# Optimization experiments

Hardware: AMD Instinct MI355X
Metric: run time of the kernel (lower is better)

## Reference

```python
import jax, jax.numpy as jnp
import numpy as np

B, T, D_IN, H, K, C = 8, 2048, 512, 384, 8192, 8
N_BLOCKS = 6
EPS = 1e-5


def conv1d(x, w, b, pad, groups=1):
    # x: [B, Cin, T], w: [Cout, Cin//groups, k]
    y = jax.lax.conv_general_dilated(
        x, w, window_strides=(1,), padding=[(pad, pad)],
        dimension_numbers=("NCH", "OIH", "NCH"), feature_group_count=groups)
    return y + b[None, :, None]


def layernorm(x, g, b):
    # normalize over last axis
    m = jnp.mean(x, axis=-1, keepdims=True)
    v = jnp.mean(jnp.square(x - m), axis=-1, keepdims=True)
    return (x - m) * jax.lax.rsqrt(v + EPS) * g + b


def setup_inputs() -> dict:
    key = jax.random.key(0)
    ks = iter(jax.random.split(key, 32))
    s = 0.02
    inp = {
        "x": jax.random.normal(next(ks), (B, T, D_IN), dtype=jnp.float32),
        "enc_w": jax.random.normal(next(ks), (H, D_IN, 7)) * s,
        "enc_b": jnp.zeros((H,)),
        "enc_ln_g": jnp.ones((H,)),
        "enc_ln_b": jnp.zeros((H,)),
        "blk_dw_w": jax.random.normal(next(ks), (N_BLOCKS, H, 1, 7)) * s,
        "blk_dw_b": jnp.zeros((N_BLOCKS, H)),
        "blk_ln_g": jnp.ones((N_BLOCKS, H)),
        "blk_ln_b": jnp.zeros((N_BLOCKS, H)),
        "blk_w1": jax.random.normal(next(ks), (N_BLOCKS, 4 * H, H)) * s,
        "blk_b1": jnp.zeros((N_BLOCKS, 4 * H)),
        "blk_w2": jax.random.normal(next(ks), (N_BLOCKS, H, 4 * H)) * s,
        "blk_b2": jnp.zeros((N_BLOCKS, H)),
        "out_w": jax.random.normal(next(ks), (C, H, 1)) * s,
        "out_b": jnp.zeros((C,)),
        "embeddings": jax.random.normal(next(ks), (K, C)),
    }
    return inp


def encode(x, enc_w, enc_b, enc_ln_g, enc_ln_b, blk_dw_w, blk_dw_b,
           blk_ln_g, blk_ln_b, blk_w1, blk_b1, blk_w2, blk_b2, out_w, out_b):
    h = x.transpose(0, 2, 1)                       # [B, D_IN, T]
    h = conv1d(h, enc_w, enc_b, pad=3)             # [B, H, T]
    h = layernorm(h.transpose(0, 2, 1), enc_ln_g, enc_ln_b).transpose(0, 2, 1)
    for i in range(N_BLOCKS):
        res = h
        h = conv1d(h, blk_dw_w[i], blk_dw_b[i], pad=3, groups=H)  # depthwise
        ht = h.transpose(0, 2, 1)                  # [B, T, H]
        ht = layernorm(ht, blk_ln_g[i], blk_ln_b[i])
        ht = jnp.einsum("bth,fh->btf", ht, blk_w1[i]) + blk_b1[i]
        ht = jax.nn.gelu(ht, approximate=False)    # torch GELU is exact erf
        ht = jnp.einsum("btf,hf->bth", ht, blk_w2[i]) + blk_b2[i]
        h = ht.transpose(0, 2, 1) + res
    z = conv1d(h, out_w, out_b, pad=0)             # [B, C, T]
    return z.transpose(0, 2, 1)                    # [B, T, C]


def reference(x, enc_w, enc_b, enc_ln_g, enc_ln_b, blk_dw_w, blk_dw_b,
              blk_ln_g, blk_ln_b, blk_w1, blk_b1, blk_w2, blk_b2,
              out_w, out_b, embeddings):
    z = encode(x, enc_w, enc_b, enc_ln_g, enc_ln_b, blk_dw_w, blk_dw_b,
               blk_ln_g, blk_ln_b, blk_w1, blk_b1, blk_w2, blk_b2, out_w, out_b)
    flat = z.reshape(-1, C)                        # [B*T, C]
    # squared euclidean distances: same argmin as torch.cdist
    d2 = (jnp.sum(flat * flat, axis=1, keepdims=True)
          - 2.0 * flat @ embeddings.T
          + jnp.sum(embeddings * embeddings, axis=1))  # [B*T, K]
    indices = jnp.argmin(d2, axis=1)               # [B*T], int
    return indices
```

## Files before the change

kernel.cpp:

```cpp
#include <hip/hip_runtime.h>
#include <math.h>

#define T_   2048
#define DIN  512
#define H_   384
#define H4_  1536
#define BT_  16384

typedef _Float16 half_t;
typedef _Float16 f16x8 __attribute__((ext_vector_type(8)));
typedef float f32x4 __attribute__((ext_vector_type(4)));

#define LO_SCALE 2048.0f
#define LO_INV   4.8828125e-4f

#define APLANE 4096
#define BPLANE 2048
#define ASL_OFF 8192
#define BSH_OFF 16384
#define BSL_OFF 20480
#define SMEM_H  24576

__device__ __forceinline__ void lds_barrier() {
    asm volatile("s_waitcnt lgkmcnt(0)\n\ts_barrier" ::: "memory");
}

__device__ __forceinline__ void split2(float v, half_t* hi, half_t* lo) {
    half_t h = (half_t)v;
    *hi = h;
    *lo = (half_t)((v - (float)h) * LO_SCALE);
}

__global__ void k_split(const float* __restrict__ in, half_t* __restrict__ hi,
                        half_t* __restrict__ lo, long n) {
    long i = (long)blockIdx.x * 256 + threadIdx.x;
    if (i >= n) return;
    split2(in[i], hi + i, lo + i);
}

__global__ void k_split_encw(const float* __restrict__ in, half_t* __restrict__ hi,
                             half_t* __restrict__ lo) {
    int idx = blockIdx.x * 256 + threadIdx.x;
    if (idx >= H_ * 3584) return;
    int n = idx / 3584;
    int r = idx % 3584;
    int tap = r >> 9, i = r & 511;
    split2(in[n * 3584 + i * 7 + tap], hi + idx, lo + idx);
}

__global__ void k_ln(const float* __restrict__ in, float* __restrict__ out,
                     const float* __restrict__ g, const float* __restrict__ b) {
    int row = blockIdx.x;
    int lane = threadIdx.x;
    const float* ir = in + (long)row * H_;
    float v[6];
    float s = 0.f;
#pragma unroll
    for (int j = 0; j < 6; ++j) { v[j] = ir[lane + (j << 6)]; s += v[j]; }
#pragma unroll
    for (int o = 32; o > 0; o >>= 1) s += __shfl_down(s, o, 64);
    s = __shfl(s, 0, 64);
    float mean = s * (1.f / 384.f);
    float q = 0.f;
#pragma unroll
    for (int j = 0; j < 6; ++j) { float d = v[j] - mean; q += d * d; }
#pragma unroll
    for (int o = 32; o > 0; o >>= 1) q += __shfl_down(q, o, 64);
    q = __shfl(q, 0, 64);
    float rstd = rsqrtf(q * (1.f / 384.f) + 1e-5f);
    float* orow = out + (long)row * H_;
#pragma unroll
    for (int j = 0; j < 6; ++j) {
        int c = lane + (j << 6);
        orow[c] = (v[j] - mean) * rstd * g[c] + b[c];
    }
}

__global__ __launch_bounds__(256) void k_dwconv_ln(
    const float* __restrict__ h, half_t* __restrict__ oh,
    half_t* __restrict__ ol,
    const float* __restrict__ w, const float* __restrict__ wb,
    const float* __restrict__ g, const float* __restrict__ gb) {
    int row = (blockIdx.x << 2) + (threadIdx.x >> 6);
    int b = row >> 11;
    int t = row & 2047;
    int lane = threadIdx.x & 63;
    const float* hb = h + ((long)b * T_) * H_;
    float v[6];
    float s = 0.f;
#pragma unroll
    for (int j = 0; j < 6; ++j) {
        int c = lane + (j << 6);
        float acc = wb[c];
        const float* wc = w + c * 7;
#pragma unroll
        for (int k = 0; k < 7; ++k) {
            int tt = t + k - 3;
            if ((unsigned)tt < (unsigned)T_)
                acc = fmaf(hb[(long)tt * H_ + c], wc[k], acc);
        }
        v[j] = acc;
        s += acc;
    }
#pragma unroll
    for (int o = 32; o > 0; o >>= 1) s += __shfl_down(s, o, 64);
    s = __shfl(s, 0, 64);
    float mean = s * (1.f / 384.f);
    float q = 0.f;
#pragma unroll
    for (int j = 0; j < 6; ++j) { float d = v[j] - mean; q += d * d; }
#pragma unroll
    for (int o = 32; o > 0; o >>= 1) q += __shfl_down(q, o, 64);
    q = __shfl(q, 0, 64);
    float rstd = rsqrtf(q * (1.f / 384.f) + 1e-5f);
    long ro = (long)row * H_;
#pragma unroll
    for (int j = 0; j < 6; ++j) {
        int c = lane + (j << 6);
        float val = (v[j] - mean) * rstd * g[c] + gb[c];
        split2(val, oh + ro + c, ol + ro + c);
    }
}

template <int MODE>
__global__ __launch_bounds__(256) void k_mgemm(
    const half_t* __restrict__ Ah, const half_t* __restrict__ Al,
    const half_t* __restrict__ Bh, const half_t* __restrict__ Bl,
    const float* __restrict__ bias, const float* __restrict__ res,
    float* __restrict__ Cf, half_t* __restrict__ Ch, half_t* __restrict__ Cl,
    int N, int K) {
    __shared__ __align__(16) half_t smem[SMEM_H];
    const int tid = threadIdx.x;
    const int lane = tid & 63, wid = tid >> 6;
    const int wm = (wid >> 1) << 6, wn = (wid & 1) << 5;
    const int quad = lane >> 4, l16 = lane & 15;
    const int m0 = (MODE == 0 ? blockIdx.x : blockIdx.y) << 7;
    const int n0 = (MODE == 0 ? blockIdx.y : blockIdx.x) << 6;
    const int ar = tid >> 2;
    const int ak = (tid & 3) << 3;
    const int br = tid >> 2, bk = (tid & 3) << 3;

    long aoff0 = 0, aoff1 = 0;
    int tt0 = 0, tt1 = 0, bq = 0;
    if (MODE == 0) {
        bq = m0 >> 11;
        tt0 = (m0 & 2047) + ar - 3;
        tt1 = tt0 + 64;
    } else {
        aoff0 = (long)(m0 + ar) * K + ak;
        aoff1 = aoff0 + (long)64 * K;
    }
    const long boff = (long)(n0 + br) * K + bk;

    float4 pa0h, pa0l, pa1h, pa1l, pbh, pbl;
    auto loadregs = [&](int k0) {
        if (MODE == 0) {
            int kk = k0 + ak;
            int tap = kk >> 9, ii = kk & 511;
            int ta = tt0 + tap, tb = tt1 + tap;
            pa0h = pa0l = pa1h = pa1l = make_float4(0.f, 0.f, 0.f, 0.f);
            if ((unsigned)ta < 2048u) {
                long o = ((long)bq * 2048 + ta) * 512 + ii;
                pa0h = *(const float4*)(Ah + o);
                pa0l = *(const float4*)(Al + o);
            }
            if ((unsigned)tb < 2048u) {
                long o = ((long)bq * 2048 + tb) * 512 + ii;
                pa1h = *(const float4*)(Ah + o);
                pa1l = *(const float4*)(Al + o);
            }
        } else {
            pa0h = *(const float4*)(Ah + aoff0 + k0);
            pa0l = *(const float4*)(Al + aoff0 + k0);
            pa1h = *(const float4*)(Ah + aoff1 + k0);
            pa1l = *(const float4*)(Al + aoff1 + k0);
        }
        pbh = *(const float4*)(Bh + boff + k0);
        pbl = *(const float4*)(Bl + boff + k0);
    };
    const int aw = ar * 32 + ((((tid & 3) ^ ar) & 3) << 3);
    const int bw = br * 32 + ((((tid & 3) ^ br) & 3) << 3);
    auto storebuf = [&](int buf) {
        int a = buf * APLANE + aw;
        *(float4*)&smem[a] = pa0h;
        *(float4*)&smem[a + 2048] = pa1h;
        int al = ASL_OFF + buf * APLANE + aw;
        *(float4*)&smem[al] = pa0l;
        *(float4*)&smem[al + 2048] = pa1l;
        *(float4*)&smem[BSH_OFF + buf * BPLANE + bw] = pbh;
        *(float4*)&smem[BSL_OFF + buf * BPLANE + bw] = pbl;
    };

    f32x4 acc1[4][2] = {};
    f32x4 acc2[4][2] = {};

    loadregs(0);
    storebuf(0);
    const int nIter = K >> 5;
    int cur = 0;
    const int sw = ((quad ^ l16) & 3) << 3;
    for (int it = 0; it < nIter; ++it) {
        if (it + 1 < nIter) loadregs((it + 1) << 5);
        lds_barrier();
        const int ab = cur * APLANE + (wm + l16) * 32 + sw;
        const int bb = BSH_OFF + cur * BPLANE + (wn + l16) * 32 + sw;
        f16x8 fah[4], fal[4], fgh[2], fgl[2];
#pragma unroll
        for (int f = 0; f < 4; ++f) {
            fah[f] = *(const f16x8*)&smem[ab + f * 512];
            fal[f] = *(const f16x8*)&smem[ab + ASL_OFF + f * 512];
        }
#pragma unroll
        for (int g = 0; g < 2; ++g) {
            fgh[g] = *(const f16x8*)&smem[bb + g * 512];
            fgl[g] = *(const f16x8*)&smem[bb + 4096 + g * 512];
        }
#pragma unroll
        for (int f = 0; f < 4; ++f)
#pragma unroll
            for (int g = 0; g < 2; ++g)
                acc2[f][g] = __builtin_amdgcn_mfma_f32_16x16x32_f16(fah[f], fgl[g], acc2[f][g], 0, 0, 0);
#pragma unroll
        for (int f = 0; f < 4; ++f)
#pragma unroll
            for (int g = 0; g < 2; ++g)
                acc2[f][g] = __builtin_amdgcn_mfma_f32_16x16x32_f16(fal[f], fgh[g], acc2[f][g], 0, 0, 0);
#pragma unroll
        for (int f = 0; f < 4; ++f)
#pragma unroll
            for (int g = 0; g < 2; ++g)
                acc1[f][g] = __builtin_amdgcn_mfma_f32_16x16x32_f16(fah[f], fgh[g], acc1[f][g], 0, 0, 0);
        if (it + 1 < nIter) storebuf(cur ^ 1);
        cur ^= 1;
    }

    float bv[2];
    bv[0] = bias[n0 + wn + l16];
    bv[1] = bias[n0 + wn + 16 + l16];

    if (MODE == 1) {
        __syncthreads();
#pragma unroll
        for (int f = 0; f < 4; ++f)
#pragma unroll
            for (int g = 0; g < 2; ++g)
#pragma unroll
                for (int r = 0; r < 4; ++r) {
                    int rm = wm + f * 16 + quad * 4 + r;
                    int cn = wn + g * 16 + l16;
                    float v = acc1[f][g][r] + acc2[f][g][r] * LO_INV + bv[g];
                    v = 0.5f * v * (1.0f + erff(v * 0.70710678118654752f));
                    half_t hh = (half_t)v;
                    smem[rm * 72 + cn] = hh;
                    smem[9216 + rm * 72 + cn] = (half_t)((v - (float)hh) * LO_SCALE);
                }
        __syncthreads();
#pragma unroll
        for (int s = 0; s < 4; ++s) {
            int idx = tid + (s << 8);
            int row = idx >> 3, c8 = (idx & 7) << 3;
            long go = (long)(m0 + row) * N + n0 + c8;
            *(float4*)(Ch + go) = *(const float4*)&smem[row * 72 + c8];
            *(float4*)(Cl + go) = *(const float4*)&smem[9216 + row * 72 + c8];
        }
    } else {
#pragma unroll
        for (int f = 0; f < 4; ++f)
#pragma unroll
            for (int g = 0; g < 2; ++g)
#pragma unroll
                for (int r = 0; r < 4; ++r) {
                    long row = m0 + wm + f * 16 + quad * 4 + r;
                    int col = n0 + wn + g * 16 + l16;
                    float v = acc1[f][g][r] + acc2[f][g][r] * LO_INV + bv[g];
                    long o = row * N + col;
                    if (MODE == 2) v += res[o];
                    Cf[o] = v;
                }
    }
}

__global__ __launch_bounds__(256) void k_outconv_argmin(
    const float* __restrict__ h, const float* __restrict__ ow,
    const float* __restrict__ ob, const float* __restrict__ emb,
    int* __restrict__ outIdx) {
    __shared__ float hs[16][H_ + 1];
    __shared__ float zs[16][8];
    __shared__ float es[16 * 516];
    __shared__ float rb[16][16];
    __shared__ int ri[16][16];
    const int tid = threadIdx.x;
    const int row0 = blockIdx.x << 4;

    for (int i = tid; i < 16 * (H_ / 4); i += 256) {
        int r = i / 96;
        int c4 = (i % 96) << 2;
        float4 v = *(const float4*)&h[((long)(row0 + r)) * H_ + c4];
        hs[r][c4] = v.x; hs[r][c4 + 1] = v.y; hs[r][c4 + 2] = v.z; hs[r][c4 + 3] = v.w;
    }
    __syncthreads();

    if (tid < 128) {
        int r = tid & 15, c = tid >> 4;
        float acc = ob[c];
        const float* wc = ow + c * H_;
        for (int j = 0; j < H_; ++j) acc = fmaf(hs[r][j], wc[j], acc);
        zs[r][c] = acc;
    }
    __syncthreads();

    const int r = tid & 15;
    const int sl = tid >> 4;
    float z0 = zs[r][0], z1 = zs[r][1], z2 = zs[r][2], z3 = zs[r][3];
    float z4 = zs[r][4], z5 = zs[r][5], z6 = zs[r][6], z7 = zs[r][7];
    float best = 3.4e38f;
    int bi = 0;

    for (int ch = 0; ch < 8; ++ch) {
        __syncthreads();
        for (int i = tid; i < 2048; i += 256) {
            int e = i >> 1;
            int half = (i & 1) << 2;
            float4 src = *(const float4*)&emb[(((long)(ch << 10)) + e) * 8 + half];
            *(float4*)&es[(e >> 6) * 516 + ((e & 63) << 3) + half] = src;
        }
        __syncthreads();
        const float* ep = es + sl * 516;
        int gbase = (ch << 10) + (sl << 6);
#pragma unroll 4
        for (int j = 0; j < 64; ++j) {
            float4 e0 = *(const float4*)(ep + (j << 3));
            float4 e1 = *(const float4*)(ep + (j << 3) + 4);
            float t, d;
            t = e0.x - z0; d = t * t;
            t = e0.y - z1; d = fmaf(t, t, d);
            t = e0.z - z2; d = fmaf(t, t, d);
            t = e0.w - z3; d = fmaf(t, t, d);
            t = e1.x - z4; d = fmaf(t, t, d);
            t = e1.y - z5; d = fmaf(t, t, d);
            t = e1.z - z6; d = fmaf(t, t, d);
            t = e1.w - z7; d = fmaf(t, t, d);
            if (d < best) { best = d; bi = gbase + j; }
        }
    }
    rb[r][sl] = best;
    ri[r][sl] = bi;
    __syncthreads();
    if (sl == 0) {
        float bb = rb[r][0];
        int bbi = ri[r][0];
#pragma unroll
        for (int s2 = 1; s2 < 16; ++s2) {
            float v = rb[r][s2];
            int i2 = ri[r][s2];
            if (v < bb || (v == bb && i2 < bbi)) { bb = v; bbi = i2; }
        }
        outIdx[row0 + r] = bbi;
    }
}

extern "C" void kernel_launch(void* const* d_in, const int* in_sizes, int n_in,
                              void* d_out, int out_size, void* d_ws, size_t ws_size,
                              hipStream_t stream) {
    const float* x        = (const float*)d_in[0];
    const float* enc_w    = (const float*)d_in[1];
    const float* enc_b    = (const float*)d_in[2];
    const float* enc_ln_g = (const float*)d_in[3];
    const float* enc_ln_b = (const float*)d_in[4];
    const float* blk_dw_w = (const float*)d_in[5];
    const float* blk_dw_b = (const float*)d_in[6];
    const float* blk_ln_g = (const float*)d_in[7];
    const float* blk_ln_b = (const float*)d_in[8];
    const float* blk_w1   = (const float*)d_in[9];
    const float* blk_b1   = (const float*)d_in[10];
    const float* blk_w2   = (const float*)d_in[11];
    const float* blk_b2   = (const float*)d_in[12];
    const float* out_w    = (const float*)d_in[13];
    const float* out_b    = (const float*)d_in[14];
    const float* emb      = (const float*)d_in[15];
    int* out = (int*)d_out;

    char* base = (char*)d_ws;
    float*  h    = (float*)base;
    half_t* tmph = (half_t*)(base + 25165824);
    half_t* tmpl = (half_t*)(base + 37748736);
    half_t* ht4h = (half_t*)(base + 50331648);
    half_t* ht4l = (half_t*)(base + 100663296);
    half_t* ench = (half_t*)(base + 150994944);
    half_t* encl = (half_t*)(base + 153747456);
    half_t* w1h  = (half_t*)(base + 156499968);
    half_t* w1l  = (half_t*)(base + 163577856);
    half_t* w2h  = (half_t*)(base + 170655744);
    half_t* w2l  = (half_t*)(base + 177733632);
    half_t* xh = ht4h;
    half_t* xl = (half_t*)(base + 50331648 + 16777216);

    k_split<<<(8388608 + 255) / 256, 256, 0, stream>>>(x, xh, xl, 8388608L);
    k_split<<<(3538944 + 255) / 256, 256, 0, stream>>>(blk_w1, w1h, w1l, 3538944L);
    k_split<<<(3538944 + 255) / 256, 256, 0, stream>>>(blk_w2, w2h, w2l, 3538944L);
    k_split_encw<<<(H_ * 3584 + 255) / 256, 256, 0, stream>>>(enc_w, ench, encl);

    k_mgemm<0><<<dim3(128, 6), 256, 0, stream>>>(xh, xl, ench, encl, enc_b,
                                                 nullptr, h, nullptr, nullptr,
                                                 H_, 3584);
    k_ln<<<BT_, 64, 0, stream>>>(h, h, enc_ln_g, enc_ln_b);

    for (int i = 0; i < 6; ++i) {
        k_dwconv_ln<<<BT_ / 4, 256, 0, stream>>>(h, tmph, tmpl, blk_dw_w + i * H_ * 7,
                                                 blk_dw_b + i * H_, blk_ln_g + i * H_,
                                                 blk_ln_b + i * H_);
        k_mgemm<1><<<dim3(24, 128), 256, 0, stream>>>(
            tmph, tmpl, w1h + (long)i * 589824, w1l + (long)i * 589824,
            blk_b1 + i * H4_, nullptr, nullptr, ht4h, ht4l, H4_, H_);
        k_mgemm<2><<<dim3(6, 128), 256, 0, stream>>>(
            ht4h, ht4l, w2h + (long)i * 589824, w2l + (long)i * 589824,
            blk_b2 + i * H_, h, h, nullptr, nullptr, H_, H4_);
    }

    k_outconv_argmin<<<BT_ / 16, 256, 0, stream>>>(h, out_w, out_b, emb, out);
}
```

Before: 1.886 ms.

## Enlarge GEMM block tile to 128x128 with 512 threads and 8 waves

```diff
diff --git a/kernel.cpp b/kernel.cpp
--- a/kernel.cpp
+++ b/kernel.cpp
@@ -15,11 +15,10 @@
 #define LO_INV   4.8828125e-4f
 
 #define APLANE 4096
-#define BPLANE 2048
 #define ASL_OFF 8192
 #define BSH_OFF 16384
-#define BSL_OFF 20480
-#define SMEM_H  24576
+#define BSL_OFF 24576
+#define SMEM_H  32768
 
 __device__ __forceinline__ void lds_barrier() {
     asm volatile("s_waitcnt lgkmcnt(0)\n\ts_barrier" ::: "memory");
@@ -123,7 +122,7 @@
 }
 
 template <int MODE>
-__global__ __launch_bounds__(256) void k_mgemm(
+__global__ __launch_bounds__(512) void k_mgemm(
     const half_t* __restrict__ Ah, const half_t* __restrict__ Al,
     const half_t* __restrict__ Bh, const half_t* __restrict__ Bl,
     const float* __restrict__ bias, const float* __restrict__ res,
@@ -132,63 +131,49 @@
     __shared__ __align__(16) half_t smem[SMEM_H];
     const int tid = threadIdx.x;
     const int lane = tid & 63, wid = tid >> 6;
-    const int wm = (wid >> 1) << 6, wn = (wid & 1) << 5;
+    const int wm = (wid >> 2) << 6, wn = (wid & 3) << 5;
     const int quad = lane >> 4, l16 = lane & 15;
     const int m0 = (MODE == 0 ? blockIdx.x : blockIdx.y) << 7;
-    const int n0 = (MODE == 0 ? blockIdx.y : blockIdx.x) << 6;
+    const int n0 = (MODE == 0 ? blockIdx.y : blockIdx.x) << 7;
     const int ar = tid >> 2;
     const int ak = (tid & 3) << 3;
-    const int br = tid >> 2, bk = (tid & 3) << 3;
-
-    long aoff0 = 0, aoff1 = 0;
-    int tt0 = 0, tt1 = 0, bq = 0;
+
+    long aoff = 0;
+    int tt0 = 0, bq = 0;
     if (MODE == 0) {
         bq = m0 >> 11;
         tt0 = (m0 & 2047) + ar - 3;
-        tt1 = tt0 + 64;
     } else {
-        aoff0 = (long)(m0 + ar) * K + ak;
-        aoff1 = aoff0 + (long)64 * K;
-    }
-    const long boff = (long)(n0 + br) * K + bk;
-
-    float4 pa0h, pa0l, pa1h, pa1l, pbh, pbl;
+        aoff = (long)(m0 + ar) * K + ak;
+    }
+    const long boff = (long)(n0 + ar) * K + ak;
+
+    float4 pAh, pAl, pBh, pBl;
     auto loadregs = [&](int k0) {
         if (MODE == 0) {
             int kk = k0 + ak;
             int tap = kk >> 9, ii = kk & 511;
-            int ta = tt0 + tap, tb = tt1 + tap;
-            pa0h = pa0l = pa1h = pa1l = make_float4(0.f, 0.f, 0.f, 0.f);
+            int ta = tt0 + tap;
+            pAh = pAl = make_float4(0.f, 0.f, 0.f, 0.f);
             if ((unsigned)ta < 2048u) {
                 long o = ((long)bq * 2048 + ta) * 512 + ii;
-                pa0h = *(const float4*)(Ah + o);
-                pa0l = *(const float4*)(Al + o);
-            }
-            if ((unsigned)tb < 2048u) {
-                long o = ((long)bq * 2048 + tb) * 512 + ii;
-                pa1h = *(const float4*)(Ah + o);
-                pa1l = *(const float4*)(Al + o);
+                pAh = *(const float4*)(Ah + o);
+                pAl = *(const float4*)(Al + o);
             }
         } else {
-            pa0h = *(const float4*)(Ah + aoff0 + k0);
-            pa0l = *(const float4*)(Al + aoff0 + k0);
-            pa1h = *(const float4*)(Ah + aoff1 + k0);
-            pa1l = *(const float4*)(Al + aoff1 + k0);
-        }
-        pbh = *(const float4*)(Bh + boff + k0);
-        pbl = *(const float4*)(Bl + boff + k0);
+            pAh = *(const float4*)(Ah + aoff + k0);
+            pAl = *(const float4*)(Al + aoff + k0);
+        }
+        pBh = *(const float4*)(Bh + boff + k0);
+        pBl = *(const float4*)(Bl + boff + k0);
     };
     const int aw = ar * 32 + ((((tid & 3) ^ ar) & 3) << 3);
-    const int bw = br * 32 + ((((tid & 3) ^ br) & 3) << 3);
     auto storebuf = [&](int buf) {
         int a = buf * APLANE + aw;
-        *(float4*)&smem[a] = pa0h;
-        *(float4*)&smem[a + 2048] = pa1h;
-        int al = ASL_OFF + buf * APLANE + aw;
-        *(float4*)&smem[al] = pa0l;
-        *(float4*)&smem[al + 2048] = pa1l;
-        *(float4*)&smem[BSH_OFF + buf * BPLANE + bw] = pbh;
-        *(float4*)&smem[BSL_OFF + buf * BPLANE + bw] = pbl;
+        *(float4*)&smem[a] = pAh;
+        *(float4*)&smem[a + ASL_OFF] = pAl;
+        *(float4*)&smem[a + BSH_OFF] = pBh;
+        *(float4*)&smem[a + BSL_OFF] = pBl;
     };
 
     f32x4 acc1[4][2] = {};
@@ -203,7 +188,7 @@
         if (it + 1 < nIter) loadregs((it + 1) << 5);
         lds_barrier();
         const int ab = cur * APLANE + (wm + l16) * 32 + sw;
-        const int bb = BSH_OFF + cur * BPLANE + (wn + l16) * 32 + sw;
+        const int bb = BSH_OFF + cur * APLANE + (wn + l16) * 32 + sw;
         f16x8 fah[4], fal[4], fgh[2], fgl[2];
 #pragma unroll
         for (int f = 0; f < 4; ++f) {
@@ -213,7 +198,7 @@
 #pragma unroll
         for (int g = 0; g < 2; ++g) {
             fgh[g] = *(const f16x8*)&smem[bb + g * 512];
-            fgl[g] = *(const f16x8*)&smem[bb + 4096 + g * 512];
+            fgl[g] = *(const f16x8*)&smem[bb + ASL_OFF + g * 512];
         }
 #pragma unroll
         for (int f = 0; f < 4; ++f)
@@ -239,29 +224,33 @@
     bv[1] = bias[n0 + wn + 16 + l16];
 
     if (MODE == 1) {
-        __syncthreads();
-#pragma unroll
-        for (int f = 0; f < 4; ++f)
-#pragma unroll
-            for (int g = 0; g < 2; ++g)
-#pragma unroll
-                for (int r = 0; r < 4; ++r) {
-                    int rm = wm + f * 16 + quad * 4 + r;
-                    int cn = wn + g * 16 + l16;
-                    float v = acc1[f][g][r] + acc2[f][g][r] * LO_INV + bv[g];
-                    v = 0.5f * v * (1.0f + erff(v * 0.70710678118654752f));
-                    half_t hh = (half_t)v;
-                    smem[rm * 72 + cn] = hh;
-                    smem[9216 + rm * 72 + cn] = (half_t)((v - (float)hh) * LO_SCALE);
-                }
-        __syncthreads();
-#pragma unroll
-        for (int s = 0; s < 4; ++s) {
-            int idx = tid + (s << 8);
-            int row = idx >> 3, c8 = (idx & 7) << 3;
-            long go = (long)(m0 + row) * N + n0 + c8;
-            *(float4*)(Ch + go) = *(const float4*)&smem[row * 72 + c8];
-            *(float4*)(Cl + go) = *(const float4*)&smem[9216 + row * 72 + c8];
+#pragma unroll
+        for (int h2 = 0; h2 < 2; ++h2) {
+            __syncthreads();
+            if (((wid >> 1) & 1) == h2) {
+                int cbase = (wid & 1) << 5;
+#pragma unroll
+                for (int f = 0; f < 4; ++f)
+#pragma unroll
+                    for (int g = 0; g < 2; ++g)
+#pragma unroll
+                        for (int r = 0; r < 4; ++r) {
+                            int rm = wm + f * 16 + quad * 4 + r;
+                            int cn = cbase + g * 16 + l16;
+                            float v = acc1[f][g][r] + acc2[f][g][r] * LO_INV + bv[g];
+                            v = 0.5f * v * (1.0f + erff(v * 0.70710678118654752f));
+                            half_t hh = (half_t)v;
+                            smem[rm * 72 + cn] = hh;
+                            smem[9216 + rm * 72 + cn] = (half_t)((v - (float)hh) * LO_SCALE);
+                        }
+            }
+            __syncthreads();
+            int row = tid >> 2, c16 = (tid & 3) << 4;
+            long go = (long)(m0 + row) * N + n0 + (h2 << 6) + c16;
+            *(float4*)(Ch + go)     = *(const float4*)&smem[row * 72 + c16];
+            *(float4*)(Ch + go + 8) = *(const float4*)&smem[row * 72 + c16 + 8];
+            *(float4*)(Cl + go)     = *(const float4*)&smem[9216 + row * 72 + c16];
+            *(float4*)(Cl + go + 8) = *(const float4*)&smem[9216 + row * 72 + c16 + 8];
         }
     } else {
 #pragma unroll
@@ -400,7 +389,7 @@
     k_split<<<(3538944 + 255) / 256, 256, 0, stream>>>(blk_w2, w2h, w2l, 3538944L);
     k_split_encw<<<(H_ * 3584 + 255) / 256, 256, 0, stream>>>(enc_w, ench, encl);
 
-    k_mgemm<0><<<dim3(128, 6), 256, 0, stream>>>(xh, xl, ench, encl, enc_b,
+    k_mgemm<0><<<dim3(128, 3), 512, 0, stream>>>(xh, xl, ench, encl, enc_b,
                                                  nullptr, h, nullptr, nullptr,
                                                  H_, 3584);
     k_ln<<<BT_, 64, 0, stream>>>(h, h, enc_ln_g, enc_ln_b);
@@ -409,10 +398,10 @@
         k_dwconv_ln<<<BT_ / 4, 256, 0, stream>>>(h, tmph, tmpl, blk_dw_w + i * H_ * 7,
                                                  blk_dw_b + i * H_, blk_ln_g + i * H_,
                                                  blk_ln_b + i * H_);
-        k_mgemm<1><<<dim3(24, 128), 256, 0, stream>>>(
+        k_mgemm<1><<<dim3(12, 128), 512, 0, stream>>>(
             tmph, tmpl, w1h + (long)i * 589824, w1l + (long)i * 589824,
             blk_b1 + i * H4_, nullptr, nullptr, ht4h, ht4l, H4_, H_);
-        k_mgemm<2><<<dim3(6, 128), 256, 0, stream>>>(
+        k_mgemm<2><<<dim3(3, 128), 512, 0, stream>>>(
             ht4h, ht4l, w2h + (long)i * 589824, w2l + (long)i * 589824,
             blk_b2 + i * H_, h, h, nullptr, nullptr, H_, H4_);
     }
```

Result: no change. 1.850 ms (-1.9%).
